# Kernel tuning notes

Measured on AMD Instinct MI355X. Metric: run time of the kernel, lower is better.

The kernel has to match this reference:

```python
import jax, jax.numpy as jnp
import numpy as np

N, E = 50000, 250000          # nodes, edges
IN, OUT, EDIM = 9, 84, 1      # NNConv(9, 84), edge nn Linear(1, 9*84)
EPS = 1e-5                    # BatchNorm1d default eps


def setup_inputs() -> dict:
    key = jax.random.key(0)
    ks = jax.random.split(key, 8)
    return {
        "x": jax.random.normal(ks[0], (N, IN), jnp.float32),
        "edge_index": jax.random.randint(ks[1], (2, E), 0, N, dtype=jnp.int64),
        "edge_attr": jax.random.normal(ks[2], (E, EDIM), jnp.float32),
        # edge nn: Linear(EDIM, IN*OUT) generating per-edge weight matrices
        "nn_w": jax.random.normal(ks[3], (EDIM, IN * OUT), jnp.float32) * (1.0 / np.sqrt(EDIM)),
        "nn_b": jnp.zeros((IN * OUT,), jnp.float32),
        # NNConv root weight + bias
        "root": jax.random.normal(ks[4], (IN, OUT), jnp.float32) * (1.0 / np.sqrt(IN)),
        "bias": jnp.zeros((OUT,), jnp.float32),
        # BatchNorm1d(84) affine params
        "gamma": jnp.ones((OUT,), jnp.float32),
        "beta": jnp.zeros((OUT,), jnp.float32),
    }


def reference(x, edge_index, edge_attr, nn_w, nn_b, root, bias, gamma, beta):
    src, dst = edge_index[0], edge_index[1]
    # per-edge weight matrices: [E, IN, OUT]
    w_e = (edge_attr @ nn_w + nn_b).reshape(E, IN, OUT)
    # gather source node features and apply edge-specific matmul: [E, OUT]
    msg = jnp.einsum('ei,eio->eo', x[src], w_e)
    # scatter-add to destination nodes (NNConv default aggr='add'): [N, OUT]
    aggr = jax.ops.segment_sum(msg, dst, num_segments=N)
    out = x @ root + aggr + bias
    # BatchNorm1d(84), training mode (biased batch stats)
    mean = out.mean(0)
    var = out.var(0)
    out = (out - mean) * jax.lax.rsqrt(var + EPS) * gamma + beta
    return out
```

## Files before the change

kernel.cpp:

```cpp
#include <hip/hip_runtime.h>

#define N_NODES 50000
#define E_EDGES 250000
#define IN_F 9
#define OUT_F 84
#define GROUPS 21
#define BN_EPS 1e-5f

#define NB_TILE 48
#define NTILES ((N_NODES + NB_TILE - 1) / NB_TILE)
#define NCOPIES 32
#define CAP 32

#define VDIM 27
#define NPAIR 378
#define NM 405
#define SLEN 408
#define VSTR 52
#define NSLOT 196

#define CNT_OFF   0
#define STATC_OFF 50048
#define ZERO_WORDS 63104
#define SLOT_OFF  63232
#define S_OFF     3263232
#define SS_OFF    4163232

__global__ __launch_bounds__(256)
void fill_slots_kernel(const int* __restrict__ ei,
                       const float* __restrict__ ea,
                       int* __restrict__ cnt,
                       int2* __restrict__ slot) {
    int e = (blockIdx.x * blockDim.x + threadIdx.x) * 4;
    if (e < E_EDGES) {
        int4   s4 = *(const int4*)&ei[e];
        int4   d4 = *(const int4*)&ei[E_EDGES + e];
        float4 a4 = *(const float4*)&ea[e];
        int pos;
        pos = atomicAdd(&cnt[d4.x], 1);
        if (pos < CAP) slot[d4.x * CAP + pos] = make_int2(s4.x, __float_as_int(a4.x));
        pos = atomicAdd(&cnt[d4.y], 1);
        if (pos < CAP) slot[d4.y * CAP + pos] = make_int2(s4.y, __float_as_int(a4.y));
        pos = atomicAdd(&cnt[d4.z], 1);
        if (pos < CAP) slot[d4.z * CAP + pos] = make_int2(s4.z, __float_as_int(a4.z));
        pos = atomicAdd(&cnt[d4.w], 1);
        if (pos < CAP) slot[d4.w * CAP + pos] = make_int2(s4.w, __float_as_int(a4.w));
    }
}

__global__ void gather_gram_kernel(const float* __restrict__ x,
                                   const int*   __restrict__ cnt,
                                   const int2*  __restrict__ slot,
                                   float* __restrict__ S,
                                   float* __restrict__ statc) {
    __shared__ __align__(16) float V[VDIM * VSTR];
    __shared__ __align__(16) int2 rec[NB_TILE][CAP];
    __shared__ int cnt_s[NB_TILE];
    __shared__ unsigned char sI[NSLOT], sJ[NSLOT];

    const int tid = threadIdx.x;
    const int nbase = blockIdx.x * NB_TILE;

    for (int t = tid; t < NSLOT; t += blockDim.x) {
        int tt = t, i = 0;
        while (tt >= ((VDIM - i + 1) >> 1)) { tt -= (VDIM - i + 1) >> 1; ++i; }
        sI[t] = (unsigned char)i;
        sJ[t] = (unsigned char)(i + 2 * tt);
    }
    for (int t = tid; t < VDIM * 4; t += blockDim.x)
        V[(t >> 2) * VSTR + NB_TILE + (t & 3)] = 0.f;
    if (tid < NB_TILE) {
        int n = nbase + tid;
        int c = (n < N_NODES) ? cnt[n] : 0;
        cnt_s[tid] = (c > CAP) ? CAP : c;
    }
    __syncthreads();

    if (tid < NB_TILE * 4) {
        int nl = tid >> 2, part = tid & 3;
        int c = cnt_s[nl];
        const int4* grow = (const int4*)&slot[(nbase + nl) * CAP];
        int4* lrow = (int4*)&rec[nl][0];
#pragma unroll
        for (int j = 0; j < 4; ++j) {
            int s = part * 8 + j * 2;
            if (s < c) lrow[part * 4 + j] = grow[part * 4 + j];
        }
    }
    __syncthreads();

    for (int it = tid; it < NB_TILE * IN_F; it += blockDim.x) {
        int nl = it / IN_F, i = it - nl * IN_F;
        int n = nbase + nl;
        float xv = 0.f, s0 = 0.f, s1 = 0.f;
        if (n < N_NODES) {
            xv = x[n * IN_F + i];
            int c = cnt_s[nl];
            const int2* r = rec[nl];
            int k = 0;
            for (; k + 4 <= c; k += 4) {
                int2 r0 = r[k], r1 = r[k+1], r2 = r[k+2], r3 = r[k+3];
                float a0 = x[r0.x * IN_F + i];
                float a1 = x[r1.x * IN_F + i];
                float a2 = x[r2.x * IN_F + i];
                float a3 = x[r3.x * IN_F + i];
                s0 += (a0 + a1) + (a2 + a3);
                s1 += __int_as_float(r0.y) * a0 + __int_as_float(r1.y) * a1
                    + __int_as_float(r2.y) * a2 + __int_as_float(r3.y) * a3;
            }
            for (; k < c; ++k) {
                int2 r0 = r[k];
                float a0 = x[r0.x * IN_F + i];
                s0 += a0;
                s1 += __int_as_float(r0.y) * a0;
            }
            S[n * 18 + i]     = s0;
            S[n * 18 + 9 + i] = s1;
        }
        V[i * VSTR + nl]        = xv;
        V[(9 + i) * VSTR + nl]  = s0;
        V[(18 + i) * VSTR + nl] = s1;
    }
    __syncthreads();

    float* sc = statc + (blockIdx.x & (NCOPIES - 1)) * SLEN;
    for (int t = tid; t < NSLOT + VDIM; t += blockDim.x) {
        if (t < NSLOT) {
            int i = sI[t], j0 = sJ[t];
            int h2 = (j0 < VDIM - 1);
            const float4* vi = (const float4*)&V[i * VSTR];
            const float4* va = (const float4*)&V[j0 * VSTR];
            const float4* vb = (const float4*)&V[(j0 + h2) * VSTR];
            float acc0 = 0.f, acc1 = 0.f;
#pragma unroll
            for (int m = 0; m < VSTR / 4; ++m) {
                float4 a = vi[m], p = va[m], q = vb[m];
                acc0 += a.x * p.x + a.y * p.y + a.z * p.z + a.w * p.w;
                acc1 += a.x * q.x + a.y * q.y + a.z * q.z + a.w * q.w;
            }
            int base = i * VDIM - (i * (i - 1)) / 2;
            atomicAdd(&sc[base + (j0 - i)], acc0);
            if (h2) atomicAdd(&sc[base + (j0 - i) + 1], acc1);
        } else {
            int r = t - NSLOT;
            const float4* vi = (const float4*)&V[r * VSTR];
            float acc = 0.f;
#pragma unroll
            for (int m = 0; m < VSTR / 4; ++m) {
                float4 a = vi[m];
                acc += (a.x + a.y) + (a.z + a.w);
            }
            atomicAdd(&sc[NPAIR + r], acc);
        }
    }
}

__global__ __launch_bounds__(256)
void scale_kernel(const float* __restrict__ nw,
                  const float* __restrict__ nb,
                  const float* __restrict__ root,
                  const float* __restrict__ bias,
                  const float* __restrict__ gamma,
                  const float* __restrict__ beta,
                  const float* __restrict__ statc,
                  float* __restrict__ ss) {
    __shared__ float M[NM];
    const int tid = threadIdx.x;
    for (int t = tid; t < NM; t += blockDim.x) {
        float a = 0.f;
#pragma unroll
        for (int c = 0; c < NCOPIES; ++c) a += statc[c * SLEN + t];
        M[t] = a;
    }
    __syncthreads();
    if (tid < OUT_F) {
        const int o = tid;
        float c[VDIM];
#pragma unroll
        for (int i = 0; i < IN_F; ++i) {
            c[i]      = root[i * OUT_F + o];
            c[9 + i]  = nb[i * OUT_F + o];
            c[18 + i] = nw[i * OUT_F + o];
        }
        float sv = 0.f;
#pragma unroll
        for (int i = 0; i < VDIM; ++i) sv += M[NPAIR + i] * c[i];
        float q = 0.f;
        int t2 = 0;
        for (int i = 0; i < VDIM; ++i) {
            q += c[i] * c[i] * M[t2++];
            for (int j = i + 1; j < VDIM; ++j)
                q += 2.f * c[i] * c[j] * M[t2++];
        }
        const float b = bias[o];
        const float inv_n = 1.0f / (float)N_NODES;
        float mean  = (sv + (float)N_NODES * b) * inv_n;
        float sumsq = q + 2.f * b * sv + (float)N_NODES * b * b;
        float var   = sumsq * inv_n - mean * mean;
        float scl   = rsqrtf(var + BN_EPS) * gamma[o];
        ss[o]         = scl;
        ss[OUT_F + o] = beta[o] - mean * scl;
    }
}

__global__ __launch_bounds__(256)
void final_kernel(const float* __restrict__ x,
                  const float* __restrict__ S,
                  const float* __restrict__ nw,
                  const float* __restrict__ nb,
                  const float* __restrict__ root,
                  const float* __restrict__ bias,
                  const float* __restrict__ ss,
                  float* __restrict__ out) {
    __shared__ __align__(16) float4 Ws[IN_F * GROUPS];
    __shared__ __align__(16) float4 Bs[IN_F * GROUPS];
    __shared__ __align__(16) float4 Rs[IN_F * GROUPS];
    __shared__ __align__(16) float4 bs4[GROUPS];
    __shared__ __align__(16) float ssl[2 * OUT_F];
    __shared__ float Xt[NB_TILE * IN_F];
    __shared__ float St[NB_TILE * 18];

    const int tid = threadIdx.x;
    const int nbase = blockIdx.x * NB_TILE;

    for (int t = tid; t < IN_F * GROUPS; t += blockDim.x) {
        Ws[t] = ((const float4*)nw)[t];
        Bs[t] = ((const float4*)nb)[t];
        Rs[t] = ((const float4*)root)[t];
    }
    if (tid < GROUPS) bs4[tid] = ((const float4*)bias)[tid];
    if (tid < 2 * OUT_F) ssl[tid] = ss[tid];

    for (int it = tid; it < NB_TILE * IN_F; it += blockDim.x) {
        int nl = it / IN_F, i = it - nl * IN_F;
        int n = nbase + nl;
        float xv = 0.f, s0 = 0.f, s1 = 0.f;
        if (n < N_NODES) {
            xv = x[n * IN_F + i];
            s0 = S[n * 18 + i];
            s1 = S[n * 18 + 9 + i];
        }
        Xt[nl * IN_F + i]   = xv;
        St[nl * 18 + i]     = s0;
        St[nl * 18 + 9 + i] = s1;
    }
    __syncthreads();

    const int g = tid % GROUPS;
    if (tid < 252) {
        float4 sc4 = *(const float4*)&ssl[g * 4];
        float4 sh4 = *(const float4*)&ssl[OUT_F + g * 4];
#pragma unroll
        for (int k = 0; k < 4; ++k) {
            int p  = tid + k * 252;
            int nl = p / GROUPS;
            int n  = nbase + nl;
            if (n < N_NODES) {
                float4 acc = bs4[g];
#pragma unroll
                for (int i = 0; i < IN_F; ++i) {
                    float xv = Xt[nl * IN_F + i];
                    float s0 = St[nl * 18 + i];
                    float s1 = St[nl * 18 + 9 + i];
                    float4 r = Rs[i * GROUPS + g];
                    float4 w = Ws[i * GROUPS + g];
                    float4 b = Bs[i * GROUPS + g];
                    acc.x += xv * r.x + s1 * w.x + s0 * b.x;
                    acc.y += xv * r.y + s1 * w.y + s0 * b.y;
                    acc.z += xv * r.z + s1 * w.z + s0 * b.z;
                    acc.w += xv * r.w + s1 * w.w + s0 * b.w;
                }
                acc.x = acc.x * sc4.x + sh4.x;
                acc.y = acc.y * sc4.y + sh4.y;
                acc.z = acc.z * sc4.z + sh4.z;
                acc.w = acc.w * sc4.w + sh4.w;
                *(float4*)&out[n * OUT_F + g * 4] = acc;
            }
        }
    }
}

extern "C" void kernel_launch(void* const* d_in, const int* in_sizes, int n_in,
                              void* d_out, int out_size, void* d_ws, size_t ws_size,
                              hipStream_t stream) {
    const float* x     = (const float*)d_in[0];
    const int*   ei    = (const int*)d_in[1];
    const float* ea    = (const float*)d_in[2];
    const float* nw    = (const float*)d_in[3];
    const float* nb    = (const float*)d_in[4];
    const float* root  = (const float*)d_in[5];
    const float* bias  = (const float*)d_in[6];
    const float* gamma = (const float*)d_in[7];
    const float* beta  = (const float*)d_in[8];
    float*       out   = (float*)d_out;

    float* wsf   = (float*)d_ws;
    int*   wsi   = (int*)d_ws;
    int*   cnt   = wsi + CNT_OFF;
    float* statc = wsf + STATC_OFF;
    int2*  slot  = (int2*)(wsi + SLOT_OFF);
    float* S     = wsf + S_OFF;
    float* ss    = wsf + SS_OFF;

    hipMemsetAsync(wsi, 0, ZERO_WORDS * sizeof(int), stream);
    fill_slots_kernel<<<(E_EDGES / 4 + 255) / 256, 256, 0, stream>>>(ei, ea, cnt, slot);
    gather_gram_kernel<<<NTILES, 256, 0, stream>>>(x, cnt, slot, S, statc);
    scale_kernel<<<1, 256, 0, stream>>>(nw, nb, root, bias, gamma, beta, statc, ss);
    final_kernel<<<NTILES, 256, 0, stream>>>(x, S, nw, nb, root, bias, ss, out);
}
```

Baseline: 120.5 us.

## Register-cache per-group weights and vectorize tile loads in final kernel

Result: faster. 116.5 us (-3.4%).

```diff
diff --git a/kernel.cpp b/kernel.cpp
--- a/kernel.cpp
+++ b/kernel.cpp
@@ -18,6 +18,10 @@
 #define SLEN 408
 #define VSTR 52
 #define NSLOT 196
+
+#define FB_TILE 96
+#define FB_NT ((N_NODES + FB_TILE - 1) / FB_TILE)
+#define VTS 28
 
 #define CNT_OFF   0
 #define STATC_OFF 50048
@@ -203,7 +207,7 @@
     }
 }
 
-__global__ __launch_bounds__(256)
+__global__ __launch_bounds__(256, 2)
 void final_kernel(const float* __restrict__ x,
                   const float* __restrict__ S,
                   const float* __restrict__ nw,
@@ -215,61 +219,92 @@
     __shared__ __align__(16) float4 Ws[IN_F * GROUPS];
     __shared__ __align__(16) float4 Bs[IN_F * GROUPS];
     __shared__ __align__(16) float4 Rs[IN_F * GROUPS];
-    __shared__ __align__(16) float4 bs4[GROUPS];
-    __shared__ __align__(16) float ssl[2 * OUT_F];
-    __shared__ float Xt[NB_TILE * IN_F];
-    __shared__ float St[NB_TILE * 18];
+    __shared__ __align__(16) float Vt[FB_TILE * VTS];
 
     const int tid = threadIdx.x;
-    const int nbase = blockIdx.x * NB_TILE;
+    const int nbase = blockIdx.x * FB_TILE;
+    const int nn = (N_NODES - nbase < FB_TILE) ? (N_NODES - nbase) : FB_TILE;
 
     for (int t = tid; t < IN_F * GROUPS; t += blockDim.x) {
         Ws[t] = ((const float4*)nw)[t];
         Bs[t] = ((const float4*)nb)[t];
         Rs[t] = ((const float4*)root)[t];
     }
-    if (tid < GROUPS) bs4[tid] = ((const float4*)bias)[tid];
-    if (tid < 2 * OUT_F) ssl[tid] = ss[tid];
-
-    for (int it = tid; it < NB_TILE * IN_F; it += blockDim.x) {
-        int nl = it / IN_F, i = it - nl * IN_F;
-        int n = nbase + nl;
-        float xv = 0.f, s0 = 0.f, s1 = 0.f;
-        if (n < N_NODES) {
-            xv = x[n * IN_F + i];
-            s0 = S[n * 18 + i];
-            s1 = S[n * 18 + 9 + i];
-        }
-        Xt[nl * IN_F + i]   = xv;
-        St[nl * 18 + i]     = s0;
-        St[nl * 18 + 9 + i] = s1;
+
+    {
+        const float4* xs = (const float4*)(x + nbase * IN_F);
+        const int nf4 = (nn * IN_F) >> 2;
+        for (int f = tid; f < nf4; f += blockDim.x) {
+            float4 v = xs[f];
+            int fl = f * 4;
+            int nl0 = fl / 9,       i0 = fl - nl0 * 9;
+            int nl1 = (fl + 1) / 9, i1 = (fl + 1) - nl1 * 9;
+            int nl2 = (fl + 2) / 9, i2 = (fl + 2) - nl2 * 9;
+            int nl3 = (fl + 3) / 9, i3 = (fl + 3) - nl3 * 9;
+            Vt[nl0 * VTS + i0] = v.x;
+            Vt[nl1 * VTS + i1] = v.y;
+            Vt[nl2 * VTS + i2] = v.z;
+            Vt[nl3 * VTS + i3] = v.w;
+        }
+    }
+    {
+        const float4* s4 = (const float4*)(S + nbase * 18);
+        const int nf4 = (nn * 18) >> 2;
+        for (int f = tid; f < nf4; f += blockDim.x) {
+            float4 v = s4[f];
+            int fl = f * 4;
+            int nl0 = fl / 18,       j0 = fl - nl0 * 18;
+            int nl1 = (fl + 1) / 18, j1 = (fl + 1) - nl1 * 18;
+            int nl2 = (fl + 2) / 18, j2 = (fl + 2) - nl2 * 18;
+            int nl3 = (fl + 3) / 18, j3 = (fl + 3) - nl3 * 18;
+            Vt[nl0 * VTS + 9 + j0] = v.x;
+            Vt[nl1 * VTS + 9 + j1] = v.y;
+            Vt[nl2 * VTS + 9 + j2] = v.z;
+            Vt[nl3 * VTS + 9 + j3] = v.w;
+        }
     }
     __syncthreads();
 
     const int g = tid % GROUPS;
+    const int lane = tid / GROUPS;
     if (tid < 252) {
-        float4 sc4 = *(const float4*)&ssl[g * 4];
-        float4 sh4 = *(const float4*)&ssl[OUT_F + g * 4];
-#pragma unroll
-        for (int k = 0; k < 4; ++k) {
-            int p  = tid + k * 252;
-            int nl = p / GROUPS;
-            int n  = nbase + nl;
+        float4 C[27];
+#pragma unroll
+        for (int i = 0; i < IN_F; ++i) {
+            C[i]      = Rs[i * GROUPS + g];
+            C[9 + i]  = Bs[i * GROUPS + g];
+            C[18 + i] = Ws[i * GROUPS + g];
+        }
+        const float4 b4  = ((const float4*)bias)[g];
+        const float4 sc4 = ((const float4*)ss)[g];
+        const float4 sh4 = ((const float4*)(ss + OUT_F))[g];
+#pragma unroll
+        for (int k = 0; k < 8; ++k) {
+            const int nl = k * 12 + lane;
+            const int n  = nbase + nl;
             if (n < N_NODES) {
-                float4 acc = bs4[g];
-#pragma unroll
-                for (int i = 0; i < IN_F; ++i) {
-                    float xv = Xt[nl * IN_F + i];
-                    float s0 = St[nl * 18 + i];
-                    float s1 = St[nl * 18 + 9 + i];
-                    float4 r = Rs[i * GROUPS + g];
-                    float4 w = Ws[i * GROUPS + g];
-                    float4 b = Bs[i * GROUPS + g];
-                    acc.x += xv * r.x + s1 * w.x + s0 * b.x;
-                    acc.y += xv * r.y + s1 * w.y + s0 * b.y;
-                    acc.z += xv * r.z + s1 * w.z + s0 * b.z;
-                    acc.w += xv * r.w + s1 * w.w + s0 * b.w;
-                }
+                const float* vr = &Vt[nl * VTS];
+                float4 a0 = *(const float4*)(vr + 0);
+                float4 a1 = *(const float4*)(vr + 4);
+                float4 a2 = *(const float4*)(vr + 8);
+                float4 a3 = *(const float4*)(vr + 12);
+                float4 a4 = *(const float4*)(vr + 16);
+                float4 a5 = *(const float4*)(vr + 20);
+                float4 a6 = *(const float4*)(vr + 24);
+                float4 acc = b4;
+#define ACC(VC, IDX)                                                      \
+                acc.x += (VC) * C[IDX].x;                                 \
+                acc.y += (VC) * C[IDX].y;                                 \
+                acc.z += (VC) * C[IDX].z;                                 \
+                acc.w += (VC) * C[IDX].w;
+                ACC(a0.x, 0)  ACC(a0.y, 1)  ACC(a0.z, 2)  ACC(a0.w, 3)
+                ACC(a1.x, 4)  ACC(a1.y, 5)  ACC(a1.z, 6)  ACC(a1.w, 7)
+                ACC(a2.x, 8)  ACC(a2.y, 9)  ACC(a2.z, 10) ACC(a2.w, 11)
+                ACC(a3.x, 12) ACC(a3.y, 13) ACC(a3.z, 14) ACC(a3.w, 15)
+                ACC(a4.x, 16) ACC(a4.y, 17) ACC(a4.z, 18) ACC(a4.w, 19)
+                ACC(a5.x, 20) ACC(a5.y, 21) ACC(a5.z, 22) ACC(a5.w, 23)
+                ACC(a6.x, 24) ACC(a6.y, 25) ACC(a6.z, 26)
+#undef ACC
                 acc.x = acc.x * sc4.x + sh4.x;
                 acc.y = acc.y * sc4.y + sh4.y;
                 acc.z = acc.z * sc4.z + sh4.z;
@@ -306,5 +341,5 @@
     fill_slots_kernel<<<(E_EDGES / 4 + 255) / 256, 256, 0, stream>>>(ei, ea, cnt, slot);
     gather_gram_kernel<<<NTILES, 256, 0, stream>>>(x, cnt, slot, S, statc);
     scale_kernel<<<1, 256, 0, stream>>>(nw, nb, root, bias, gamma, beta, statc, ss);
-    final_kernel<<<NTILES, 256, 0, stream>>>(x, S, nw, nb, root, bias, ss, out);
-}
+    final_kernel<<<FB_NT, 256, 0, stream>>>(x, S, nw, nb, root, bias, ss, out);
+}
```
